# Performance work log

Hardware: AMD Instinct MI355X
Metric: run time of the kernel (lower is better)

The kernel has to match this reference:

```python
import jax, jax.numpy as jnp
import numpy as np


def setup_inputs() -> dict:
    key = jax.random.key(0)
    ks = jax.random.split(key, 5)
    B, N, Fin, Fout = 8, 2048, 512, 512
    stdv = 1.0 / np.sqrt(Fout)
    w_stdv = 1.0 / np.sqrt(Fin)
    x = jax.random.normal(ks[0], (B, N, Fin), dtype=jnp.float32)
    weight = jax.random.uniform(ks[1], (Fin, Fout), dtype=jnp.float32, minval=-stdv, maxval=stdv)
    bias = jax.random.uniform(ks[2], (Fout,), dtype=jnp.float32, minval=-stdv, maxval=stdv)
    w_one = jax.random.uniform(ks[3], (Fin, Fin), dtype=jnp.float32, minval=-w_stdv, maxval=w_stdv)
    w_two = jax.random.uniform(ks[4], (Fin, Fin), dtype=jnp.float32, minval=-w_stdv, maxval=w_stdv)
    return {"x": x, "weight": weight, "bias": bias, "w_one": w_one, "w_two": w_two}


def reference(x, weight, bias, w_one, w_two):
    # x: [B, N, Fin]
    support = jnp.einsum('bnf,fo->bno', x, weight)          # [B, N, Fout]
    phi_one = jnp.einsum('ef,bnf->ben', w_one, x)           # [B, Fin, N]
    phi_two = jnp.einsum('ef,bnf->ben', w_two, x)           # [B, Fin, N]
    adj = jnp.einsum('ben,bem->bnm', phi_one, phi_two)      # [B, N, N]
    adj = jax.nn.softmax(adj, axis=1)                        # softmax over dim=1 (columns)
    out = jnp.einsum('bnm,bmo->bno', adj, support)           # [B, N, Fout]
    return out + bias
```

## Files before the change

kernel.cpp:

```cpp
#include <hip/hip_runtime.h>
#include <math.h>

#define BB 8
#define NN 2048
#define FF 512
#define LOG2E 1.4426950408889634f

typedef __attribute__((ext_vector_type(8))) short short8;
typedef __attribute__((ext_vector_type(4))) float floatx4;
typedef __attribute__((ext_vector_type(2))) float float2v;
typedef __attribute__((ext_vector_type(2))) __bf16 bf16x2;

__device__ __forceinline__ unsigned short f2bf(float f) {
    union { float f; unsigned u; } v; v.f = f;
    unsigned r = v.u + 0x7FFFu + ((v.u >> 16) & 1u);
    return (unsigned short)(r >> 16);
}

__device__ __forceinline__ float fexp2(float x) {
#if __has_builtin(__builtin_amdgcn_exp2f)
    return __builtin_amdgcn_exp2f(x);
#else
    return __expf(x * 0.69314718056f);
#endif
}

__device__ __forceinline__ void pk_store(unsigned short* p0, unsigned short* p1,
                                         float a, float b) {
    union { bf16x2 h; unsigned short s[2]; } u;
    float2v v; v.x = a; v.y = b;
    u.h = __builtin_convertvector(v, bf16x2);
    *p0 = u.s[0]; *p1 = u.s[1];
}

#define BAR() __builtin_amdgcn_s_barrier()
#define LGKM0() do { asm volatile("s_waitcnt lgkmcnt(0)" ::: "memory"); \
                     __builtin_amdgcn_sched_barrier(0); } while (0)
#define GLDS(src, dst) __builtin_amdgcn_global_load_lds( \
    (const __attribute__((address_space(1))) void*)(src), \
    (__attribute__((address_space(3))) void*)(dst), 16, 0, 0)
#define VMW(n) asm volatile("s_waitcnt vmcnt(" #n ")" ::: "memory")

template<int M_REP, int MODE>
__global__ __launch_bounds__(512) void gemm256(
    const unsigned short* __restrict__ A, const unsigned short* __restrict__ B,
    void* __restrict__ Cv, const float* __restrict__ bias, float* __restrict__ Dsum,
    int K, int a_ld, int b_ld, int ldc,
    long a_batch, long b_batch, long c_batch)
{
    constexpr int BM    = M_REP * 32;
    constexpr int LA    = BM / 128;
    constexpr int ASLOT = BM * 32;
    constexpr int BSLOT = 256 * 32;
    __shared__ __align__(16) unsigned short SH[4 * ASLOT + 4 * BSLOT];

    const int tid  = threadIdx.x;
    const int wave = tid >> 6;
    const int lane = tid & 63;
    const int wr   = wave >> 2;
    const int wc   = wave & 3;
    const int fl   = lane & 15;
    const int quad = lane >> 4;

    const int gx = gridDim.x, gy = gridDim.y;
    int flat = blockIdx.x + gx * (blockIdx.y + gy * blockIdx.z);
    const int cpx = (gx * gy * gridDim.z) >> 3;
    if (cpx > 0) flat = (flat & 7) * cpx + (flat >> 3);
    const int bx = flat % gx;
    const int rest = flat / gx;
    const int by = rest % gy;
    const int bz = rest / gy;

    const int m0 = by * BM;
    const int n0 = bx * 256;

    const unsigned short* Aptr = A + (long)bz * a_batch + (long)m0 * a_ld;
    const unsigned short* Bptr = B + (long)bz * b_batch + (long)n0 * b_ld;

    int offA[LA], offB[2];
    #pragma unroll
    for (int i = 0; i < LA; ++i) {
        const int cl = i * 512 + tid;
        const int r = cl >> 2, s = cl & 3;
        offA[i] = r * a_ld + (s ^ ((r >> 1) & 3)) * 8;
    }
    #pragma unroll
    for (int i = 0; i < 2; ++i) {
        const int cl = i * 512 + tid;
        const int r = cl >> 2, s = cl & 3;
        offB[i] = r * b_ld + (s ^ ((r >> 1) & 3)) * 8;
    }

    const int swz = (quad ^ ((fl >> 1) & 3)) * 8;
    const int aRd = (wr * (M_REP * 16) + fl) * 32 + swz;
    const int bRd = (wc * 64 + fl) * 32 + swz;

    auto sA = [&](int kh, int db, int kb) {
        #pragma unroll
        for (int i = 0; i < LA; ++i)
            GLDS(Aptr + kb + offA[i], &SH[(kh * 2 + db) * ASLOT + (i * 512 + tid) * 8]);
    };
    auto sB = [&](int kh, int db, int kb) {
        #pragma unroll
        for (int i = 0; i < 2; ++i)
            GLDS(Bptr + kb + offB[i], &SH[4 * ASLOT + (kh * 2 + db) * BSLOT + (i * 512 + tid) * 8]);
    };

    floatx4 acc[M_REP][4] = {};
    short8 af[M_REP], bf[2];

    auto RA = [&](int kh, int db) {
        const unsigned short* b = &SH[(kh * 2 + db) * ASLOT + aRd];
        #pragma unroll
        for (int m = 0; m < M_REP; ++m) af[m] = *(const short8*)(b + m * 512);
    };
    auto RB = [&](int kh, int db, int nh) {
        const unsigned short* b = &SH[4 * ASLOT + (kh * 2 + db) * BSLOT + bRd + nh * 1024];
        bf[0] = *(const short8*)(b);
        bf[1] = *(const short8*)(b + 512);
    };
    auto MC = [&](int nh) {
        __builtin_amdgcn_s_setprio(1);
        #pragma unroll
        for (int m = 0; m < M_REP; ++m) {
            acc[m][nh * 2]     = __builtin_amdgcn_mfma_f32_16x16x32_bf16(af[m], bf[0], acc[m][nh * 2], 0, 0, 0);
            acc[m][nh * 2 + 1] = __builtin_amdgcn_mfma_f32_16x16x32_bf16(af[m], bf[1], acc[m][nh * 2 + 1], 0, 0, 0);
        }
        __builtin_amdgcn_s_setprio(0);
    };

    const int nt = K >> 6;
    const int ni = nt >> 1;

    sA(0, 0, 0);  sB(0, 0, 0);  sA(1, 0, 32); sB(1, 0, 32);
    sA(0, 1, 64); sB(0, 1, 64); sA(1, 1, 96);
    if constexpr (LA == 2) VMW(6); else VMW(4);
    BAR();

    for (int i = 0; i < ni; ++i) {
        const bool last = (i == ni - 1);
        const int kb1 = (2 * i + 1) * 64, kb2 = kb1 + 64, kb3 = kb2 + 64;

        RA(0, 0); RB(0, 0, 0);
        sB(1, 1, kb1 + 32);
        BAR(); LGKM0(); MC(0); BAR();

        RB(0, 0, 1);
        if (!last) sA(0, 0, kb2);
        BAR(); LGKM0(); MC(1); BAR();

        RA(1, 0); RB(1, 0, 0);
        if (!last) sB(0, 0, kb2);
        BAR(); LGKM0(); MC(0); BAR();

        RB(1, 0, 1);
        if (!last) {
            sA(1, 0, kb2 + 32);
            if constexpr (LA == 2) VMW(6); else VMW(4);
        } else {
            VMW(0);
        }
        BAR(); LGKM0(); MC(1); BAR();

        RA(0, 1); RB(0, 1, 0);
        if (!last) sB(1, 0, kb2 + 32);
        BAR(); LGKM0(); MC(0); BAR();

        RB(0, 1, 1);
        if (!last) sA(0, 1, kb3);
        BAR(); LGKM0(); MC(1); BAR();

        RA(1, 1); RB(1, 1, 0);
        if (!last) sB(0, 1, kb3);
        BAR(); LGKM0(); MC(0); BAR();

        RB(1, 1, 1);
        if (!last) {
            sA(1, 1, kb3 + 32);
            if constexpr (LA == 2) VMW(6); else VMW(4);
        }
        BAR(); LGKM0(); MC(1); BAR();
    }

    const int wmg = m0 + wr * (M_REP * 16);
    const int wcol = wc * 64;

    if constexpr (MODE == 0) {
        float* Cb = (float*)Cv + (long)bz * c_batch;
        #pragma unroll
        for (int n = 0; n < 4; ++n) {
            const int ng = n0 + wcol + n * 16 + fl;
            const float badd = bias ? bias[ng] : 0.0f;
            #pragma unroll
            for (int m = 0; m < M_REP; ++m) {
                const int mg = wmg + m * 16 + quad * 4;
                #pragma unroll
                for (int r = 0; r < 4; ++r)
                    Cb[(long)(mg + r) * ldc + ng] = acc[m][n][r] + badd;
            }
        }
    } else {
        unsigned short* Cb = (unsigned short*)Cv + (long)bz * c_batch;
        if constexpr (MODE == 2) {
            float* Db = Dsum + (long)bz * NN;
            #pragma unroll
            for (int m = 0; m < M_REP; ++m)
                #pragma unroll
                for (int n = 0; n < 4; ++n)
                    #pragma unroll
                    for (int r = 0; r < 4; ++r)
                        acc[m][n][r] = fexp2(acc[m][n][r]);
            #pragma unroll
            for (int n = 0; n < 4; ++n) {
                float csum = 0.f;
                #pragma unroll
                for (int m = 0; m < M_REP; ++m)
                    csum += acc[m][n][0] + acc[m][n][1] + acc[m][n][2] + acc[m][n][3];
                csum += __shfl_xor(csum, 16);
                csum += __shfl_xor(csum, 32);
                if (quad == 0) atomicAdd(&Db[n0 + wcol + n * 16 + fl], csum);
            }
        }
        __syncthreads();
        #pragma unroll
        for (int m = 0; m < M_REP; ++m) {
            const int rowb = wr * (M_REP * 16) + m * 16 + quad * 4;
            #pragma unroll
            for (int n = 0; n < 4; ++n) {
                const int pc = (wcol + n * 16 + fl) ^ (quad << 4);
                #pragma unroll
                for (int r = 0; r < 4; ++r)
                    SH[(rowb + r) * 256 + pc] = f2bf(acc[m][n][r]);
            }
        }
        __syncthreads();
        #pragma unroll
        for (int k = 0; k < M_REP * 2; ++k) {
            const int idx = k * 512 + tid;
            const int row = idx >> 5, c8 = (idx & 31) * 8;
            const int lcol = c8 ^ (((row >> 2) & 3) << 4);
            short8 vv = *(const short8*)&SH[row * 256 + lcol];
            *(short8*)&Cb[(long)(m0 + row) * ldc + n0 + c8] = vv;
        }
    }
}

__global__ __launch_bounds__(256) void gemm128_bt(
    const unsigned short* __restrict__ A, const unsigned short* __restrict__ B,
    unsigned short* __restrict__ C, int K, int a_ld, int b_ld, int ldc)
{
    __shared__ __align__(16) unsigned short Alds[128 * 64];
    __shared__ __align__(16) unsigned short Blds[128 * 64];

    const int tid  = threadIdx.x;
    const int wave = tid >> 6;
    const int lane = tid & 63;
    const int m0 = blockIdx.y * 128;
    const int n0 = blockIdx.x * 128;

    const unsigned short* Aptr = A + (long)m0 * a_ld;
    const unsigned short* Bptr = B + (long)n0 * b_ld;

    const int wm   = (wave >> 1) * 64;
    const int wn   = (wave & 1) * 64;
    const int fl   = lane & 15;
    const int quad = lane >> 4;

    int offA[4], offB[4], cb[4];
    #pragma unroll
    for (int issue = 0; issue < 4; ++issue) {
        const int cbase = issue * 256 + wave * 64;
        const int c = cbase + lane;
        const int row = c >> 3;
        const int kq = ((c & 7) ^ ((c >> 3) & 7)) * 8;
        offA[issue] = row * a_ld + kq;
        offB[issue] = row * b_ld + kq;
        cb[issue] = cbase * 8;
    }

    floatx4 acc[4][4] = {};

    for (int k0 = 0; k0 < K; k0 += 64) {
        #pragma unroll
        for (int issue = 0; issue < 4; ++issue) {
            GLDS(Aptr + offA[issue], &Alds[cb[issue] + lane * 8]);
            GLDS(Bptr + offB[issue], &Blds[cb[issue] + lane * 8]);
        }
        Aptr += 64; Bptr += 64;
        __syncthreads();

        #pragma unroll
        for (int s = 0; s < 2; ++s) {
            short8 af[4], bfr[4];
            const int slot = ((s * 4 + quad) ^ (fl & 7)) * 8;
            #pragma unroll
            for (int i = 0; i < 4; ++i)
                af[i] = *(const short8*)&Alds[(wm + i * 16 + fl) * 64 + slot];
            #pragma unroll
            for (int j = 0; j < 4; ++j)
                bfr[j] = *(const short8*)&Blds[(wn + j * 16 + fl) * 64 + slot];
            #pragma unroll
            for (int i = 0; i < 4; ++i)
                #pragma unroll
                for (int j = 0; j < 4; ++j)
                    acc[i][j] = __builtin_amdgcn_mfma_f32_16x16x32_bf16(af[i], bfr[j], acc[i][j], 0, 0, 0);
        }
        __syncthreads();
    }

    #pragma unroll
    for (int j = 0; j < 4; ++j) {
        const int ng = n0 + wn + j * 16 + fl;
        #pragma unroll
        for (int i = 0; i < 4; ++i) {
            const int mg = m0 + wm + i * 16 + quad * 4;
            pk_store(&C[(long)(mg + 0) * ldc + ng], &C[(long)(mg + 1) * ldc + ng],
                     acc[i][j][0], acc[i][j][1]);
            pk_store(&C[(long)(mg + 2) * ldc + ng], &C[(long)(mg + 3) * ldc + ng],
                     acc[i][j][2], acc[i][j][3]);
        }
    }
}

__global__ __launch_bounds__(256) void prep_all(
    const float* __restrict__ x, const float* __restrict__ w1,
    const float* __restrict__ w2, const float* __restrict__ w,
    unsigned short* __restrict__ xb, unsigned short* __restrict__ w1T,
    unsigned short* __restrict__ w2T, unsigned short* __restrict__ wT,
    float* __restrict__ Dsum)
{
    __shared__ float tl[32][33];
    int b = blockIdx.x;
    if (b < 4096) {
        const long i = ((long)b * 256 + threadIdx.x) * 8;
        float4 a = *(const float4*)(x + i);
        float4 c = *(const float4*)(x + i + 4);
        union { bf16x2 h[4]; short8 s8; } u;
        float2v v;
        v.x = a.x; v.y = a.y; u.h[0] = __builtin_convertvector(v, bf16x2);
        v.x = a.z; v.y = a.w; u.h[1] = __builtin_convertvector(v, bf16x2);
        v.x = c.x; v.y = c.y; u.h[2] = __builtin_convertvector(v, bf16x2);
        v.x = c.z; v.y = c.w; u.h[3] = __builtin_convertvector(v, bf16x2);
        *(short8*)(xb + i) = u.s8;
        return;
    }
    b -= 4096;
    if (b < 768) {
        const float* in; unsigned short* out; float sc = 1.0f;
        const int seg = b >> 8, t = b & 255;
        if (seg == 0)      { in = w1; out = w1T; sc = LOG2E; }
        else if (seg == 1) { in = w2; out = w2T; }
        else               { in = w;  out = wT; }
        const int tx = threadIdx.x & 31, ty = threadIdx.x >> 5;
        const int x0 = (t & 15) * 32, y0 = (t >> 4) * 32;
        #pragma unroll
        for (int k = 0; k < 32; k += 8)
            tl[ty + k][tx] = in[(long)(y0 + ty + k) * FF + x0 + tx];
        __syncthreads();
        #pragma unroll
        for (int k = 0; k < 32; k += 8)
            out[(long)(x0 + ty + k) * FF + y0 + tx] = f2bf(tl[tx][ty + k] * sc);
        return;
    }
    b -= 768;
    Dsum[(long)b * 256 + threadIdx.x] = 0.0f;
}

__global__ __launch_bounds__(256) void scale_transpose(
    const unsigned short* __restrict__ Call, const float* __restrict__ D,
    unsigned short* __restrict__ supT, int batch0)
{
    __shared__ float t[32][33];
    __shared__ float rD[32];
    const int tx = threadIdx.x & 31, ty = threadIdx.x >> 5;
    const int mt = blockIdx.x * 32, ot = blockIdx.y * 32;
    const int b = batch0 + blockIdx.z;
    const unsigned short* Cb = Call + (long)b * NN * 1024;
    unsigned short* Tb = supT + (long)b * NN * FF;
    if (threadIdx.x < 32) rD[threadIdx.x] = 1.0f / D[(long)b * NN + mt + threadIdx.x];
    __syncthreads();
    #pragma unroll
    for (int k = 0; k < 32; k += 8) {
        unsigned short u = Cb[(long)(mt + ty + k) * 1024 + 512 + ot + tx];
        union { unsigned uu; float f; } cv; cv.uu = ((unsigned)u) << 16;
        t[ty + k][tx] = cv.f;
    }
    __syncthreads();
    #pragma unroll
    for (int k = 0; k < 32; k += 8)
        Tb[(long)(ot + ty + k) * NN + mt + tx] = f2bf(t[tx][ty + k] * rD[tx]);
}

extern "C" void kernel_launch(void* const* d_in, const int* in_sizes, int n_in,
                              void* d_out, int out_size, void* d_ws, size_t ws_size,
                              hipStream_t stream)
{
    const float* x      = (const float*)d_in[0];
    const float* weight = (const float*)d_in[1];
    const float* bias   = (const float*)d_in[2];
    const float* w_one  = (const float*)d_in[3];
    const float* w_two  = (const float*)d_in[4];
    float* out = (float*)d_out;

    const long NF  = (long)NN * FF;
    const long NN2 = (long)NN * NN;
    const long CROW = 1024;

    char* p = (char*)d_ws;
    unsigned short* xb    = (unsigned short*)p; p += (size_t)BB * NF * 2;
    unsigned short* Wg1   = (unsigned short*)p; p += (size_t)1024 * FF * 2;
    unsigned short* w1T   = (unsigned short*)p; p += (size_t)FF * FF * 2;
    unsigned short* w2T   = (unsigned short*)p; p += (size_t)FF * FF * 2;
    unsigned short* Call  = (unsigned short*)p; p += (size_t)BB * NN * CROW * 2;
    unsigned short* supT  = (unsigned short*)p; p += (size_t)BB * NF * 2;
    float*          Dsum  = (float*)p;          p += (size_t)BB * NN * 4;
    unsigned short* E     = (unsigned short*)p;
    unsigned short* Vw  = Wg1;
    unsigned short* wTb = Wg1 + (size_t)FF * FF;

    const size_t fixed = (size_t)(p - (char*)d_ws);
    const bool full = ws_size >= fixed + (size_t)BB * NN2 * 2;

    dim3 blk(256), blk5(512);

    prep_all<<<dim3(4928), blk, 0, stream>>>(
        x, w_one, w_two, weight, xb, w1T, w2T, wTb, Dsum);

    gemm128_bt<<<dim3(FF / 128, FF / 128), blk, 0, stream>>>(
        w2T, w1T, Vw, FF, FF, FF, FF);

    gemm256<8, 1><<<dim3(1024 / 256, NN / 256, BB), blk5, 0, stream>>>(
        xb, Wg1, Call, nullptr, nullptr, FF,
        FF, FF, (int)CROW, NF, 0, NN * CROW);

    if (full) {
        gemm256<8, 2><<<dim3(NN / 256, NN / 256, BB), blk5, 0, stream>>>(
            Call, xb, E, nullptr, Dsum, FF,
            (int)CROW, FF, NN, NN * CROW, NF, NN2);
        scale_transpose<<<dim3(NN / 32, FF / 32, BB), blk, 0, stream>>>(Call, Dsum, supT, 0);
        gemm256<4, 0><<<dim3(FF / 256, NN / 128, BB), blk5, 0, stream>>>(
            E, supT, out, bias, nullptr, NN,
            NN, NN, FF, NN2, NF, NF);
    } else {
        for (int b = 0; b < BB; ++b) {
            const unsigned short* Cb = Call + (size_t)b * NN * CROW;
            gemm256<8, 2><<<dim3(NN / 256, NN / 256, 1), blk5, 0, stream>>>(
                Cb, xb + (size_t)b * NF, E, nullptr, Dsum + (size_t)b * NN, FF,
                (int)CROW, FF, NN, 0, 0, 0);
            scale_transpose<<<dim3(NN / 32, FF / 32, 1), blk, 0, stream>>>(Call, Dsum, supT, b);
            gemm256<4, 0><<<dim3(FF / 256, NN / 128, 1), blk5, 0, stream>>>(
                E, supT + (size_t)b * NF, out + (size_t)b * NF, bias, nullptr, NN,
                NN, NN, FF, 0, 0, 0);
        }
    }
}
```

Measured before the change: 214.4 us.

## Merge half-tile MFMA phases into full-tile phases with coarser prefetch

Restructures the GEMM main loop from eight half-width MFMA phases per iteration to four full-width phases. Each phase now reads all four B fragments and issues both A and B global-to-LDS prefetches together, with adjusted vmcnt waits. This halves the number of barrier pairs per iteration and gives each barrier interval more MFMA work. The cost is more live B-fragment registers and a prefetch that runs fewer phases ahead, which may expose more global load latency.

Measured after the change: 215.4 us. Within noise of the previous version (+0.5%).

```diff
diff --git a/kernel.cpp b/kernel.cpp
--- a/kernel.cpp
+++ b/kernel.cpp
@@ -107,79 +107,72 @@
     };
 
     floatx4 acc[M_REP][4] = {};
-    short8 af[M_REP], bf[2];
+    short8 af[M_REP], bf[4];
 
     auto RA = [&](int kh, int db) {
         const unsigned short* b = &SH[(kh * 2 + db) * ASLOT + aRd];
         #pragma unroll
         for (int m = 0; m < M_REP; ++m) af[m] = *(const short8*)(b + m * 512);
     };
-    auto RB = [&](int kh, int db, int nh) {
-        const unsigned short* b = &SH[4 * ASLOT + (kh * 2 + db) * BSLOT + bRd + nh * 1024];
+    auto RB4 = [&](int kh, int db) {
+        const unsigned short* b = &SH[4 * ASLOT + (kh * 2 + db) * BSLOT + bRd];
         bf[0] = *(const short8*)(b);
         bf[1] = *(const short8*)(b + 512);
+        bf[2] = *(const short8*)(b + 1024);
+        bf[3] = *(const short8*)(b + 1536);
     };
-    auto MC = [&](int nh) {
+    auto MCF = [&]() {
         __builtin_amdgcn_s_setprio(1);
         #pragma unroll
-        for (int m = 0; m < M_REP; ++m) {
-            acc[m][nh * 2]     = __builtin_amdgcn_mfma_f32_16x16x32_bf16(af[m], bf[0], acc[m][nh * 2], 0, 0, 0);
-            acc[m][nh * 2 + 1] = __builtin_amdgcn_mfma_f32_16x16x32_bf16(af[m], bf[1], acc[m][nh * 2 + 1], 0, 0, 0);
-        }
+        for (int m = 0; m < M_REP; ++m)
+            #pragma unroll
+            for (int j = 0; j < 4; ++j)
+                acc[m][j] = __builtin_amdgcn_mfma_f32_16x16x32_bf16(af[m], bf[j], acc[m][j], 0, 0, 0);
         __builtin_amdgcn_s_setprio(0);
     };
 
     const int nt = K >> 6;
     const int ni = nt >> 1;
 
-    sA(0, 0, 0);  sB(0, 0, 0);  sA(1, 0, 32); sB(1, 0, 32);
-    sA(0, 1, 64); sB(0, 1, 64); sA(1, 1, 96);
-    if constexpr (LA == 2) VMW(6); else VMW(4);
+    sA(0, 0, 0);  sB(0, 0, 0);
+    sA(1, 0, 32); sB(1, 0, 32);
+    sA(0, 1, 64); sB(0, 1, 64);
+    if constexpr (LA == 2) VMW(8); else VMW(6);
     BAR();
 
     for (int i = 0; i < ni; ++i) {
         const bool last = (i == ni - 1);
         const int kb1 = (2 * i + 1) * 64, kb2 = kb1 + 64, kb3 = kb2 + 64;
 
-        RA(0, 0); RB(0, 0, 0);
-        sB(1, 1, kb1 + 32);
-        BAR(); LGKM0(); MC(0); BAR();
-
-        RB(0, 0, 1);
-        if (!last) sA(0, 0, kb2);
-        BAR(); LGKM0(); MC(1); BAR();
-
-        RA(1, 0); RB(1, 0, 0);
-        if (!last) sB(0, 0, kb2);
-        BAR(); LGKM0(); MC(0); BAR();
-
-        RB(1, 0, 1);
+        RA(0, 0); RB4(0, 0);
+        sA(1, 1, kb1 + 32); sB(1, 1, kb1 + 32);
+        if constexpr (LA == 2) VMW(8); else VMW(6);
+        BAR(); LGKM0(); MCF(); BAR();
+
+        RA(1, 0); RB4(1, 0);
         if (!last) {
-            sA(1, 0, kb2 + 32);
-            if constexpr (LA == 2) VMW(6); else VMW(4);
+            sA(0, 0, kb2); sB(0, 0, kb2);
+            if constexpr (LA == 2) VMW(8); else VMW(6);
+        } else {
+            if constexpr (LA == 2) VMW(4); else VMW(3);
+        }
+        BAR(); LGKM0(); MCF(); BAR();
+
+        RA(0, 1); RB4(0, 1);
+        if (!last) {
+            sA(1, 0, kb2 + 32); sB(1, 0, kb2 + 32);
+            if constexpr (LA == 2) VMW(8); else VMW(6);
         } else {
             VMW(0);
         }
-        BAR(); LGKM0(); MC(1); BAR();
-
-        RA(0, 1); RB(0, 1, 0);
-        if (!last) sB(1, 0, kb2 + 32);
-        BAR(); LGKM0(); MC(0); BAR();
-
-        RB(0, 1, 1);
-        if (!last) sA(0, 1, kb3);
-        BAR(); LGKM0(); MC(1); BAR();
-
-        RA(1, 1); RB(1, 1, 0);
-        if (!last) sB(0, 1, kb3);
-        BAR(); LGKM0(); MC(0); BAR();
-
-        RB(1, 1, 1);
+        BAR(); LGKM0(); MCF(); BAR();
+
+        RA(1, 1); RB4(1, 1);
         if (!last) {
-            sA(1, 1, kb3 + 32);
-            if constexpr (LA == 2) VMW(6); else VMW(4);
-        }
-        BAR(); LGKM0(); MC(1); BAR();
+            sA(0, 1, kb3); sB(0, 1, kb3);
+            if constexpr (LA == 2) VMW(8); else VMW(6);
+        }
+        BAR(); LGKM0(); MCF(); BAR();
     }
 
     const int wmg = m0 + wr * (M_REP * 16);
```
